# Kernel tuning notes

Hardware: AMD Instinct MI355X
Metric: run time of the kernel (lower is better)

Reference implementation:

```python
import jax, jax.numpy as jnp
import numpy as np

D_MODEL = 1024
N_HEADS = 16
D_K = D_MODEL // N_HEADS


def setup_inputs() -> dict:
    key = jax.random.key(0)
    ks = jax.random.split(key, 6)
    B, T = 4, 2048
    x = jax.random.normal(ks[0], (B, T, D_MODEL), dtype=jnp.float32)
    # additive causal mask: 0 on/below diagonal, -inf above
    neg = jnp.float32(-1e9)
    attn_mask = jnp.where(jnp.tril(jnp.ones((T, T), dtype=bool)), 0.0, neg).astype(jnp.float32)
    s_in = 1.0 / np.sqrt(D_MODEL)
    Wqkv = jax.random.normal(ks[1], (D_MODEL, 3 * D_MODEL), dtype=jnp.float32) * s_in
    bqkv = jnp.zeros((3 * D_MODEL,), dtype=jnp.float32)
    Wout = jax.random.normal(ks[2], (D_MODEL, D_MODEL), dtype=jnp.float32) * s_in
    bout = jnp.zeros((D_MODEL,), dtype=jnp.float32)
    return {"x": x, "attn_mask": attn_mask, "Wqkv": Wqkv, "bqkv": bqkv,
            "Wout": Wout, "bout": bout}


def reference(x, attn_mask, Wqkv, bqkv, Wout, bout):
    B, T, _ = x.shape
    qkv = x @ Wqkv + bqkv                                  # [B,T,3*D]
    qkv = qkv.reshape(B, T, 3, N_HEADS, D_K)
    qkv = jnp.transpose(qkv, (2, 0, 3, 1, 4))              # [3,B,H,T,d_k]
    q, k, v = qkv[0], qkv[1], qkv[2]
    scores = jnp.einsum('bhqd,bhkd->bhqk', q, k) / jnp.sqrt(jnp.float32(D_K))
    scores = scores + attn_mask                            # broadcast [T,T]
    probs = jax.nn.softmax(scores, axis=-1)
    attn_out = jnp.einsum('bhqk,bhkd->bhqd', probs, v)     # [B,H,T,d_k]
    attn_out = jnp.transpose(attn_out, (0, 2, 1, 3)).reshape(B, T, D_MODEL)
    return attn_out @ Wout + bout
```

## Files before the change

kernel.cpp:

```cpp
#include <hip/hip_runtime.h>
#include <hip/hip_bf16.h>
#include <stdint.h>

typedef __attribute__((ext_vector_type(8))) short short8;
typedef __attribute__((ext_vector_type(4))) short short4v;
typedef __attribute__((ext_vector_type(4))) float f32x4;

#define MFMA16(a, b, c) __builtin_amdgcn_mfma_f32_16x16x32_bf16((a), (b), (c), 0, 0, 0)

static __device__ __forceinline__ short f2bf(float f) {
    union { float f; uint32_t i; } v; v.f = f;
    uint32_t r = v.i + 0x7fffu + ((v.i >> 16) & 1u);
    return (short)(r >> 16);
}

__global__ void conv_f32_bf16(const float* __restrict__ in, short* __restrict__ out, int n4) {
    int i = blockIdx.x * blockDim.x + threadIdx.x;
    int stride = gridDim.x * blockDim.x;
    for (; i < n4; i += stride) {
        f32x4 v = *(const f32x4*)(in + (size_t)i * 4);
        short4v o;
        o[0] = f2bf(v[0]); o[1] = f2bf(v[1]); o[2] = f2bf(v[2]); o[3] = f2bf(v[3]);
        *(short4v*)(out + (size_t)i * 4) = o;
    }
}

__global__ void conv_transpose(const float* __restrict__ W, short* __restrict__ Wt, int R, int C) {
    __shared__ float tile[32][33];
    int c0 = blockIdx.x * 32;
    int r0 = blockIdx.y * 32;
    int tx = threadIdx.x;
    int ty = threadIdx.y;
    for (int j = 0; j < 4; ++j) {
        int r = ty * 4 + j;
        tile[r][tx] = W[(size_t)(r0 + r) * C + c0 + tx];
    }
    __syncthreads();
    for (int j = 0; j < 4; ++j) {
        int c = ty * 4 + j;
        Wt[(size_t)(c0 + c) * R + r0 + tx] = f2bf(tile[tx][c]);
    }
}

__global__ __launch_bounds__(256) void gemm_qkv(
    const short* __restrict__ A, const short* __restrict__ Bt,
    const float* __restrict__ bias,
    short* __restrict__ Qg, short* __restrict__ Kg, short* __restrict__ Vg)
{
    const int K = 1024;
    __shared__ short As[128 * 32];
    __shared__ short Bs[128 * 32];
    const int tid = threadIdx.x, lane = tid & 63, wid = tid >> 6;
    const int wr = wid >> 1, wc = wid & 1;
    const int m0 = blockIdx.y * 128, n0 = blockIdx.x * 128;
    const int l15 = lane & 15, l4 = lane >> 4;

    f32x4 acc[4][4] = {};

    int rowS[2], ugS[2];
    for (int t = 0; t < 2; ++t) {
        int c = tid + t * 256;
        rowS[t] = c >> 2;
        ugS[t] = (c & 3) ^ ((rowS[t] >> 1) & 3);
    }
    int offA[4], offB[4];
    for (int f = 0; f < 4; ++f) {
        int ra = wr * 64 + f * 16 + l15;
        offA[f] = ra * 32 + ((l4 ^ ((ra >> 1) & 3)) * 8);
        int rb = wc * 64 + f * 16 + l15;
        offB[f] = rb * 32 + ((l4 ^ ((rb >> 1) & 3)) * 8);
    }

    for (int k0 = 0; k0 < K; k0 += 32) {
        __syncthreads();
        for (int t = 0; t < 2; ++t) {
            const short* ga = A  + (size_t)(m0 + rowS[t]) * K + k0 + ugS[t] * 8;
            const short* gb = Bt + (size_t)(n0 + rowS[t]) * K + k0 + ugS[t] * 8;
            short* la = As + (t * 256 + wid * 64) * 8;
            short* lb = Bs + (t * 256 + wid * 64) * 8;
            __builtin_amdgcn_global_load_lds((const __attribute__((address_space(1))) void*)ga,
                                             (__attribute__((address_space(3))) void*)la, 16, 0, 0);
            __builtin_amdgcn_global_load_lds((const __attribute__((address_space(1))) void*)gb,
                                             (__attribute__((address_space(3))) void*)lb, 16, 0, 0);
        }
        __syncthreads();
        short8 a[4], b[4];
        for (int f = 0; f < 4; ++f) a[f] = *(const short8*)&As[offA[f]];
        for (int f = 0; f < 4; ++f) b[f] = *(const short8*)&Bs[offB[f]];
        for (int mf = 0; mf < 4; ++mf)
            for (int nf = 0; nf < 4; ++nf)
                acc[mf][nf] = MFMA16(a[mf], b[nf], acc[mf][nf]);
    }

    for (int mf = 0; mf < 4; ++mf) {
        int grow_base = m0 + wr * 64 + mf * 16 + l4 * 4;
        for (int nf = 0; nf < 4; ++nf) {
            int gcol = n0 + wc * 64 + nf * 16 + l15;
            float bb = bias[gcol];
            int which = gcol >> 10, rem = gcol & 1023;
            int h = rem >> 6, d = rem & 63;
            for (int r = 0; r < 4; ++r) {
                int grow = grow_base + r;
                int b = grow >> 11, t = grow & 2047;
                int bh = (b << 4) + h;
                float val = acc[mf][nf][r] + bb;
                if (which == 0) val *= 0.125f;
                short bv = f2bf(val);
                if (which == 0)      Qg[((size_t)bh * 2048 + t) * 64 + d] = bv;
                else if (which == 1) Kg[((size_t)bh * 2048 + t) * 64 + d] = bv;
                else                 Vg[((size_t)bh * 64 + d) * 2048 + t] = bv;
            }
        }
    }
}

#define LOAD_KV(KB, VB, KV0) do {                                                               \
    _Pragma("unroll")                                                                           \
    for (int kf_ = 0; kf_ < 4; ++kf_) {                                                         \
        KB[kf_][0] = *(const short8*)&Kh[(size_t)((KV0) + kf_ * 16 + l15) * 64 + l4 * 8];       \
        KB[kf_][1] = *(const short8*)&Kh[(size_t)((KV0) + kf_ * 16 + l15) * 64 + 32 + l4 * 8];  \
        VB[kf_][0] = *(const short8*)&Vh[(size_t)(kf_ * 16 + l15) * 2048 + (KV0) + l4 * 8];     \
        VB[kf_][1] = *(const short8*)&Vh[(size_t)(kf_ * 16 + l15) * 2048 + (KV0) + 32 + l4 * 8];\
    }                                                                                           \
} while (0)

#define COMPUTE_TILE(KB, VB, KV0, DIAG) do {                                                    \
    _Pragma("unroll")                                                                           \
    for (int h_ = 0; h_ < 2; ++h_) {                                                            \
        f32x4 sf_[4];                                                                           \
        _Pragma("unroll")                                                                       \
        for (int kf_ = 0; kf_ < 4; ++kf_) {                                                     \
            f32x4 z_ = {};                                                                      \
            z_ = MFMA16(qf[h_][0], KB[kf_][0], z_);                                             \
            z_ = MFMA16(qf[h_][1], KB[kf_][1], z_);                                             \
            sf_[kf_] = z_;                                                                      \
        }                                                                                       \
        short* P_ = Pw[h_];                                                                     \
        const int gq_ = q0 + h_ * 16 + l4 * 4;                                                  \
        _Pragma("unroll")                                                                       \
        for (int kf_ = 0; kf_ < 4; ++kf_) {                                                     \
            const int gk_ = (KV0) + kf_ * 16 + l15;                                             \
            _Pragma("unroll")                                                                   \
            for (int r_ = 0; r_ < 4; ++r_) {                                                    \
                float v_ = sf_[kf_][r_];                                                        \
                if (DIAG && gk_ > gq_ + r_) v_ = -1e9f;                                         \
                float pp_ = __expf(v_);                                                         \
                lsum[h_][r_] += pp_;                                                            \
                P_[(l4 * 4 + r_) * 72 + kf_ * 16 + l15] = f2bf(pp_);                            \
            }                                                                                   \
        }                                                                                       \
        asm volatile("s_waitcnt lgkmcnt(0)" ::: "memory");                                      \
        short8 pa0_ = *(const short8*)&P_[l15 * 72 + l4 * 8];                                   \
        short8 pa1_ = *(const short8*)&P_[l15 * 72 + 32 + l4 * 8];                              \
        _Pragma("unroll")                                                                       \
        for (int df_ = 0; df_ < 4; ++df_) {                                                     \
            o[h_][df_] = MFMA16(pa0_, VB[df_][0], o[h_][df_]);                                  \
            o[h_][df_] = MFMA16(pa1_, VB[df_][1], o[h_][df_]);                                  \
        }                                                                                       \
    }                                                                                           \
} while (0)

__global__ __launch_bounds__(256, 2) void attn_kernel(
    const short* __restrict__ Qg, const short* __restrict__ Kg, const short* __restrict__ Vg,
    short* __restrict__ AO)
{
    __shared__ short Ps[4][2][16 * 72];
    const int tid = threadIdx.x, lane = tid & 63, wid = tid >> 6;
    const int l15 = lane & 15, l4 = lane >> 4;
    const int bp = blockIdx.x;
    const int xcd = bp & 7, slot = bp >> 3;
    const int bh = xcd * 8 + (slot >> 3);
    const int iblk = slot & 7;
    const int pr = iblk * 4 + wid;
    const short* Qh = Qg + (size_t)bh * 2048 * 64;
    const short* Kh = Kg + (size_t)bh * 2048 * 64;
    const short* Vh = Vg + (size_t)bh * 64 * 2048;
    const int b = bh >> 4, head = bh & 15;
    short* Pw[2] = { &Ps[wid][0][0], &Ps[wid][1][0] };

    for (int half = 0; half < 2; ++half) {
        const int s = half ? (63 - pr) : pr;
        const int q0 = s * 32;
        const int nt = (s >> 1) + 1;

        short8 qf[2][2];
        #pragma unroll
        for (int h = 0; h < 2; ++h)
            #pragma unroll
            for (int c = 0; c < 2; ++c)
                qf[h][c] = *(const short8*)&Qh[(size_t)(q0 + h * 16 + l15) * 64 + c * 32 + l4 * 8];

        f32x4 o[2][4] = {};
        float lsum[2][4] = {};

        short8 kbA[4][2], vbA[4][2], kbB[4][2], vbB[4][2];
        LOAD_KV(kbA, vbA, 0);
        int j = 0;
        for (;;) {
            if (j == nt - 1) { COMPUTE_TILE(kbA, vbA, j * 64, true); break; }
            LOAD_KV(kbB, vbB, (j + 1) * 64);
            COMPUTE_TILE(kbA, vbA, j * 64, false);
            ++j;
            if (j == nt - 1) { COMPUTE_TILE(kbB, vbB, j * 64, true); break; }
            LOAD_KV(kbA, vbA, (j + 1) * 64);
            COMPUTE_TILE(kbB, vbB, j * 64, false);
            ++j;
        }

        #pragma unroll
        for (int mk = 1; mk <= 8; mk <<= 1)
            #pragma unroll
            for (int h = 0; h < 2; ++h)
                #pragma unroll
                for (int r = 0; r < 4; ++r)
                    lsum[h][r] += __shfl_xor(lsum[h][r], mk, 64);

        #pragma unroll
        for (int h = 0; h < 2; ++h)
            #pragma unroll
            for (int r = 0; r < 4; ++r) {
                float inv = 1.0f / lsum[h][r];
                size_t grow = (size_t)b * 2048 + q0 + h * 16 + l4 * 4 + r;
                #pragma unroll
                for (int df = 0; df < 4; ++df)
                    AO[grow * 1024 + head * 64 + df * 16 + l15] = f2bf(o[h][df][r] * inv);
            }
    }
}

__global__ __launch_bounds__(256) void gemm_out(
    const short* __restrict__ A, const short* __restrict__ Bt,
    const float* __restrict__ bias, float* __restrict__ out)
{
    const int K = 1024;
    __shared__ short As[128 * 32];
    __shared__ short Bs[128 * 32];
    const int tid = threadIdx.x, lane = tid & 63, wid = tid >> 6;
    const int wr = wid >> 1, wc = wid & 1;
    const int m0 = blockIdx.y * 128, n0 = blockIdx.x * 128;
    const int l15 = lane & 15, l4 = lane >> 4;

    f32x4 acc[4][4] = {};

    int rowS[2], ugS[2];
    for (int t = 0; t < 2; ++t) {
        int c = tid + t * 256;
        rowS[t] = c >> 2;
        ugS[t] = (c & 3) ^ ((rowS[t] >> 1) & 3);
    }
    int offA[4], offB[4];
    for (int f = 0; f < 4; ++f) {
        int ra = wr * 64 + f * 16 + l15;
        offA[f] = ra * 32 + ((l4 ^ ((ra >> 1) & 3)) * 8);
        int rb = wc * 64 + f * 16 + l15;
        offB[f] = rb * 32 + ((l4 ^ ((rb >> 1) & 3)) * 8);
    }

    for (int k0 = 0; k0 < K; k0 += 32) {
        __syncthreads();
        for (int t = 0; t < 2; ++t) {
            const short* ga = A  + (size_t)(m0 + rowS[t]) * K + k0 + ugS[t] * 8;
            const short* gb = Bt + (size_t)(n0 + rowS[t]) * K + k0 + ugS[t] * 8;
            short* la = As + (t * 256 + wid * 64) * 8;
            short* lb = Bs + (t * 256 + wid * 64) * 8;
            __builtin_amdgcn_global_load_lds((const __attribute__((address_space(1))) void*)ga,
                                             (__attribute__((address_space(3))) void*)la, 16, 0, 0);
            __builtin_amdgcn_global_load_lds((const __attribute__((address_space(1))) void*)gb,
                                             (__attribute__((address_space(3))) void*)lb, 16, 0, 0);
        }
        __syncthreads();
        short8 a[4], b[4];
        for (int f = 0; f < 4; ++f) a[f] = *(const short8*)&As[offA[f]];
        for (int f = 0; f < 4; ++f) b[f] = *(const short8*)&Bs[offB[f]];
        for (int mf = 0; mf < 4; ++mf)
            for (int nf = 0; nf < 4; ++nf)
                acc[mf][nf] = MFMA16(a[mf], b[nf], acc[mf][nf]);
    }

    for (int mf = 0; mf < 4; ++mf) {
        int grow_base = m0 + wr * 64 + mf * 16 + l4 * 4;
        for (int nf = 0; nf < 4; ++nf) {
            int gcol = n0 + wc * 64 + nf * 16 + l15;
            float bb = bias[gcol];
            for (int r = 0; r < 4; ++r) {
                int grow = grow_base + r;
                out[(size_t)grow * 1024 + gcol] = acc[mf][nf][r] + bb;
            }
        }
    }
}

extern "C" void kernel_launch(void* const* d_in, const int* in_sizes, int n_in,
                              void* d_out, int out_size, void* d_ws, size_t ws_size,
                              hipStream_t stream) {
    (void)in_sizes; (void)n_in; (void)out_size; (void)ws_size;
    const float* x    = (const float*)d_in[0];
    const float* Wqkv = (const float*)d_in[2];
    const float* bqkv = (const float*)d_in[3];
    const float* Wout = (const float*)d_in[4];
    const float* bout = (const float*)d_in[5];
    float* out = (float*)d_out;

    char* ws = (char*)d_ws;
    short* xb    = (short*)(ws);
    short* WqkvT = (short*)(ws + (16ull << 20));
    short* WoutT = (short*)(ws + (22ull << 20));
    short* Qg    = (short*)(ws + (24ull << 20));
    short* Kg    = (short*)(ws + (40ull << 20));
    short* Vg    = (short*)(ws + (56ull << 20));
    short* AO    = xb;

    conv_f32_bf16<<<2048, 256, 0, stream>>>(x, xb, 8192 * 1024 / 4);
    conv_transpose<<<dim3(3072 / 32, 1024 / 32), dim3(32, 8), 0, stream>>>(Wqkv, WqkvT, 1024, 3072);
    conv_transpose<<<dim3(1024 / 32, 1024 / 32), dim3(32, 8), 0, stream>>>(Wout, WoutT, 1024, 1024);
    gemm_qkv<<<dim3(24, 64), 256, 0, stream>>>(xb, WqkvT, bqkv, Qg, Kg, Vg);
    attn_kernel<<<512, 256, 0, stream>>>(Qg, Kg, Vg, AO);
    gemm_out<<<dim3(8, 64), 256, 0, stream>>>(AO, WoutT, bout, out);
}
```

Measured before the change: 377.8 us.

## Keep attention probabilities in registers via swapped QK^T and permuted V layout

Computes S^T by swapping MFMA operands so each lane holds the probabilities in the layout needed as the A operand of the PV MFMA. V is stored with a permuted key order so that packing them with v_cvt_pk_bf16 removes the LDS round trip and waitcnt. The softmax scale now folds in log2(e) and uses exp2f, and the row-sum reduction becomes two shuffles. It also adds setprio around MFMA blocks, splits K and V loads, and optionally writes V contiguously and then runs a separate transpose kernel when the workspace is large enough. Together these cut LDS traffic and conversion cost in exchange for an extra kernel launch and more complex indexing.

```diff
diff --git a/kernel.cpp b/kernel.cpp
--- a/kernel.cpp
+++ b/kernel.cpp
@@ -5,6 +5,7 @@
 typedef __attribute__((ext_vector_type(8))) short short8;
 typedef __attribute__((ext_vector_type(4))) short short4v;
 typedef __attribute__((ext_vector_type(4))) float f32x4;
+typedef __attribute__((ext_vector_type(4))) int   i32x4;
 
 #define MFMA16(a, b, c) __builtin_amdgcn_mfma_f32_16x16x32_bf16((a), (b), (c), 0, 0, 0)
 
@@ -12,6 +13,12 @@
     union { float f; uint32_t i; } v; v.f = f;
     uint32_t r = v.i + 0x7fffu + ((v.i >> 16) & 1u);
     return (short)(r >> 16);
+}
+
+static __device__ __forceinline__ int cvtpk(float a, float b) {
+    int r;
+    asm("v_cvt_pk_bf16_f32 %0, %1, %2" : "=v"(r) : "v"(a), "v"(b));
+    return r;
 }
 
 __global__ void conv_f32_bf16(const float* __restrict__ in, short* __restrict__ out, int n4) {
@@ -45,7 +52,8 @@
 __global__ __launch_bounds__(256) void gemm_qkv(
     const short* __restrict__ A, const short* __restrict__ Bt,
     const float* __restrict__ bias,
-    short* __restrict__ Qg, short* __restrict__ Kg, short* __restrict__ Vg)
+    short* __restrict__ Qg, short* __restrict__ Kg, short* __restrict__ Vg,
+    short* __restrict__ Vc)
 {
     const int K = 1024;
     __shared__ short As[128 * 32];
@@ -104,67 +112,113 @@
                 int b = grow >> 11, t = grow & 2047;
                 int bh = (b << 4) + h;
                 float val = acc[mf][nf][r] + bb;
-                if (which == 0) val *= 0.125f;
+                if (which == 0) val *= 0.18033688011112042f;
                 short bv = f2bf(val);
                 if (which == 0)      Qg[((size_t)bh * 2048 + t) * 64 + d] = bv;
                 else if (which == 1) Kg[((size_t)bh * 2048 + t) * 64 + d] = bv;
-                else                 Vg[((size_t)bh * 64 + d) * 2048 + t] = bv;
-            }
-        }
-    }
-}
-
-#define LOAD_KV(KB, VB, KV0) do {                                                               \
+                else if (Vc)         Vc[((size_t)bh * 2048 + t) * 64 + d] = bv;
+                else {
+                    int k6 = t & 63;
+                    int pos = (k6 & 32) + ((k6 & 12) << 1) + ((k6 & 16) >> 2) + (k6 & 3);
+                    Vg[((size_t)bh * 64 + d) * 2048 + (t & ~63) + pos] = bv;
+                }
+            }
+        }
+    }
+}
+
+__global__ __launch_bounds__(256) void v_transpose(const short* __restrict__ Vc,
+                                                   short* __restrict__ Vg) {
+    __shared__ short tile[64][72];
+    const int tid = threadIdx.x;
+    const int bh = blockIdx.y;
+    const int t0 = blockIdx.x * 64;
+    {
+        int tt = tid >> 2, q = (tid & 3) * 16;
+        const short* src = Vc + ((size_t)bh * 2048 + t0 + tt) * 64 + q;
+        *(short8*)&tile[tt][q]     = *(const short8*)&src[0];
+        *(short8*)&tile[tt][q + 8] = *(const short8*)&src[8];
+    }
+    __syncthreads();
+    {
+        int d = tid >> 2, pc = (tid & 3) * 16;
+        short8 o0, o1;
+        #pragma unroll
+        for (int i = 0; i < 16; ++i) {
+            int p = pc + i;
+            int k6 = (p & 32) + ((p & 4) << 2) + ((p >> 1) & 12) + (p & 3);
+            short v = tile[k6][d];
+            if (i < 8) o0[i] = v; else o1[i - 8] = v;
+        }
+        short* dst = Vg + ((size_t)bh * 64 + d) * 2048 + t0 + pc;
+        *(short8*)&dst[0] = o0;
+        *(short8*)&dst[8] = o1;
+    }
+}
+
+#define LOADK(KB, KV0) do {                                                                     \
     _Pragma("unroll")                                                                           \
     for (int kf_ = 0; kf_ < 4; ++kf_) {                                                         \
         KB[kf_][0] = *(const short8*)&Kh[(size_t)((KV0) + kf_ * 16 + l15) * 64 + l4 * 8];       \
         KB[kf_][1] = *(const short8*)&Kh[(size_t)((KV0) + kf_ * 16 + l15) * 64 + 32 + l4 * 8];  \
-        VB[kf_][0] = *(const short8*)&Vh[(size_t)(kf_ * 16 + l15) * 2048 + (KV0) + l4 * 8];     \
-        VB[kf_][1] = *(const short8*)&Vh[(size_t)(kf_ * 16 + l15) * 2048 + (KV0) + 32 + l4 * 8];\
     }                                                                                           \
 } while (0)
 
-#define COMPUTE_TILE(KB, VB, KV0, DIAG) do {                                                    \
+#define LOADV(VB, KV0) do {                                                                     \
+    _Pragma("unroll")                                                                           \
+    for (int df_ = 0; df_ < 4; ++df_) {                                                         \
+        VB[df_][0] = *(const short8*)&Vh[(size_t)(df_ * 16 + l15) * 2048 + (KV0) + l4 * 8];     \
+        VB[df_][1] = *(const short8*)&Vh[(size_t)(df_ * 16 + l15) * 2048 + (KV0) + 32 + l4 * 8];\
+    }                                                                                           \
+} while (0)
+
+#define TILE(KB, KV0) do {                                                                      \
+    const bool diag_ = ((KV0) == (nt - 1) * 64);                                                \
     _Pragma("unroll")                                                                           \
     for (int h_ = 0; h_ < 2; ++h_) {                                                            \
         f32x4 sf_[4];                                                                           \
+        __builtin_amdgcn_s_setprio(1);                                                          \
         _Pragma("unroll")                                                                       \
         for (int kf_ = 0; kf_ < 4; ++kf_) {                                                     \
             f32x4 z_ = {};                                                                      \
-            z_ = MFMA16(qf[h_][0], KB[kf_][0], z_);                                             \
-            z_ = MFMA16(qf[h_][1], KB[kf_][1], z_);                                             \
+            z_ = MFMA16(KB[kf_][0], qf[h_][0], z_);                                             \
+            z_ = MFMA16(KB[kf_][1], qf[h_][1], z_);                                             \
             sf_[kf_] = z_;                                                                      \
         }                                                                                       \
-        short* P_ = Pw[h_];                                                                     \
-        const int gq_ = q0 + h_ * 16 + l4 * 4;                                                  \
+        __builtin_amdgcn_s_setprio(0);                                                          \
+        const int gq_ = q0 + h_ * 16 + l15;                                                     \
+        int w_[4][2];                                                                           \
         _Pragma("unroll")                                                                       \
         for (int kf_ = 0; kf_ < 4; ++kf_) {                                                     \
-            const int gk_ = (KV0) + kf_ * 16 + l15;                                             \
+            float pf_[4];                                                                       \
             _Pragma("unroll")                                                                   \
             for (int r_ = 0; r_ < 4; ++r_) {                                                    \
                 float v_ = sf_[kf_][r_];                                                        \
-                if (DIAG && gk_ > gq_ + r_) v_ = -1e9f;                                         \
-                float pp_ = __expf(v_);                                                         \
-                lsum[h_][r_] += pp_;                                                            \
-                P_[(l4 * 4 + r_) * 72 + kf_ * 16 + l15] = f2bf(pp_);                            \
+                if (diag_ && ((KV0) + kf_ * 16 + l4 * 4 + r_) > gq_) v_ = -1e9f;                \
+                float pp_ = exp2f(v_);                                                          \
+                lsum[h_] += pp_;                                                                \
+                pf_[r_] = pp_;                                                                  \
             }                                                                                   \
+            w_[kf_][0] = cvtpk(pf_[0], pf_[1]);                                                 \
+            w_[kf_][1] = cvtpk(pf_[2], pf_[3]);                                                 \
         }                                                                                       \
-        asm volatile("s_waitcnt lgkmcnt(0)" ::: "memory");                                      \
-        short8 pa0_ = *(const short8*)&P_[l15 * 72 + l4 * 8];                                   \
-        short8 pa1_ = *(const short8*)&P_[l15 * 72 + 32 + l4 * 8];                              \
+        union { i32x4 i; short8 s8; } pa0_, pa1_;                                               \
+        pa0_.i[0] = w_[0][0]; pa0_.i[1] = w_[0][1]; pa0_.i[2] = w_[1][0]; pa0_.i[3] = w_[1][1]; \
+        pa1_.i[0] = w_[2][0]; pa1_.i[1] = w_[2][1]; pa1_.i[2] = w_[3][0]; pa1_.i[3] = w_[3][1]; \
+        __builtin_amdgcn_s_setprio(1);                                                          \
         _Pragma("unroll")                                                                       \
         for (int df_ = 0; df_ < 4; ++df_) {                                                     \
-            o[h_][df_] = MFMA16(pa0_, VB[df_][0], o[h_][df_]);                                  \
-            o[h_][df_] = MFMA16(pa1_, VB[df_][1], o[h_][df_]);                                  \
+            o[h_][df_] = MFMA16(pa0_.s8, vb[df_][0], o[h_][df_]);                               \
+            o[h_][df_] = MFMA16(pa1_.s8, vb[df_][1], o[h_][df_]);                               \
         }                                                                                       \
+        __builtin_amdgcn_s_setprio(0);                                                          \
     }                                                                                           \
 } while (0)
 
-__global__ __launch_bounds__(256, 2) void attn_kernel(
+__global__ __launch_bounds__(256) void attn_kernel(
     const short* __restrict__ Qg, const short* __restrict__ Kg, const short* __restrict__ Vg,
     short* __restrict__ AO)
 {
-    __shared__ short Ps[4][2][16 * 72];
     const int tid = threadIdx.x, lane = tid & 63, wid = tid >> 6;
     const int l15 = lane & 15, l4 = lane >> 4;
     const int bp = blockIdx.x;
@@ -176,7 +230,6 @@
     const short* Kh = Kg + (size_t)bh * 2048 * 64;
     const short* Vh = Vg + (size_t)bh * 64 * 2048;
     const int b = bh >> 4, head = bh & 15;
-    short* Pw[2] = { &Ps[wid][0][0], &Ps[wid][1][0] };
 
     for (int half = 0; half < 2; ++half) {
         const int s = half ? (63 - pr) : pr;
@@ -191,35 +244,39 @@
                 qf[h][c] = *(const short8*)&Qh[(size_t)(q0 + h * 16 + l15) * 64 + c * 32 + l4 * 8];
 
         f32x4 o[2][4] = {};
-        float lsum[2][4] = {};
-
-        short8 kbA[4][2], vbA[4][2], kbB[4][2], vbB[4][2];
-        LOAD_KV(kbA, vbA, 0);
+        float lsum[2] = { 0.f, 0.f };
+
+        short8 kb0[4][2], kb1[4][2], vb[4][2];
+        LOADK(kb0, 0);
         int j = 0;
         for (;;) {
-            if (j == nt - 1) { COMPUTE_TILE(kbA, vbA, j * 64, true); break; }
-            LOAD_KV(kbB, vbB, (j + 1) * 64);
-            COMPUTE_TILE(kbA, vbA, j * 64, false);
-            ++j;
-            if (j == nt - 1) { COMPUTE_TILE(kbB, vbB, j * 64, true); break; }
-            LOAD_KV(kbA, vbA, (j + 1) * 64);
-            COMPUTE_TILE(kbB, vbB, j * 64, false);
-            ++j;
+            {
+                const int kv0 = j * 64;
+                if (j + 1 < nt) LOADK(kb1, kv0 + 64);
+                LOADV(vb, kv0);
+                TILE(kb0, kv0);
+            }
+            if (++j == nt) break;
+            {
+                const int kv0 = j * 64;
+                if (j + 1 < nt) LOADK(kb0, kv0 + 64);
+                LOADV(vb, kv0);
+                TILE(kb1, kv0);
+            }
+            if (++j == nt) break;
         }
 
         #pragma unroll
-        for (int mk = 1; mk <= 8; mk <<= 1)
-            #pragma unroll
-            for (int h = 0; h < 2; ++h)
-                #pragma unroll
-                for (int r = 0; r < 4; ++r)
-                    lsum[h][r] += __shfl_xor(lsum[h][r], mk, 64);
+        for (int h = 0; h < 2; ++h) {
+            lsum[h] += __shfl_xor(lsum[h], 16, 64);
+            lsum[h] += __shfl_xor(lsum[h], 32, 64);
+        }
 
         #pragma unroll
         for (int h = 0; h < 2; ++h)
             #pragma unroll
             for (int r = 0; r < 4; ++r) {
-                float inv = 1.0f / lsum[h][r];
+                float inv = 1.0f / __shfl(lsum[h], l4 * 4 + r, 64);
                 size_t grow = (size_t)b * 2048 + q0 + h * 16 + l4 * 4 + r;
                 #pragma unroll
                 for (int df = 0; df < 4; ++df)
@@ -293,7 +350,7 @@
 extern "C" void kernel_launch(void* const* d_in, const int* in_sizes, int n_in,
                               void* d_out, int out_size, void* d_ws, size_t ws_size,
                               hipStream_t stream) {
-    (void)in_sizes; (void)n_in; (void)out_size; (void)ws_size;
+    (void)in_sizes; (void)n_in; (void)out_size;
     const float* x    = (const float*)d_in[0];
     const float* Wqkv = (const float*)d_in[2];
     const float* bqkv = (const float*)d_in[3];
@@ -310,10 +367,14 @@
     short* Vg    = (short*)(ws + (56ull << 20));
     short* AO    = xb;
 
+    const bool coal = ws_size >= (88ull << 20);
+    short* Vc = coal ? (short*)(ws + (72ull << 20)) : (short*)nullptr;
+
     conv_f32_bf16<<<2048, 256, 0, stream>>>(x, xb, 8192 * 1024 / 4);
     conv_transpose<<<dim3(3072 / 32, 1024 / 32), dim3(32, 8), 0, stream>>>(Wqkv, WqkvT, 1024, 3072);
     conv_transpose<<<dim3(1024 / 32, 1024 / 32), dim3(32, 8), 0, stream>>>(Wout, WoutT, 1024, 1024);
-    gemm_qkv<<<dim3(24, 64), 256, 0, stream>>>(xb, WqkvT, bqkv, Qg, Kg, Vg);
+    gemm_qkv<<<dim3(24, 64), 256, 0, stream>>>(xb, WqkvT, bqkv, Qg, Kg, Vg, Vc);
+    if (coal) v_transpose<<<dim3(32, 64), 256, 0, stream>>>(Vc, Vg);
     attn_kernel<<<512, 256, 0, stream>>>(Qg, Kg, Vg, AO);
     gemm_out<<<dim3(8, 64), 256, 0, stream>>>(AO, WoutT, bout, out);
 }
```

New measurement: 1.275 ms. 3.38x slower.
